# Kernel tuning notes

Measured on AMD Instinct MI355X. Metric: run time of the kernel, lower is better.

The kernel has to match this reference:

```python
import math
import jax, jax.numpy as jnp
import numpy as np

DIM = 1024
HEADS = 16
HEAD_DIM = DIM // HEADS
NEG = -10000.0


def setup_inputs() -> dict:
    key = jax.random.key(0)
    ks = jax.random.split(key, 9)
    B, S = 2, 2048
    s = 1.0 / math.sqrt(DIM)
    inp = {
        "x": jax.random.normal(ks[0], (B, S, DIM), dtype=jnp.float32),
        "Wq": jax.random.normal(ks[1], (DIM, DIM), dtype=jnp.float32) * s,
        "bq": jnp.zeros((DIM,), dtype=jnp.float32),
        "Wk": jax.random.normal(ks[2], (DIM, DIM), dtype=jnp.float32) * s,
        "bk": jnp.zeros((DIM,), dtype=jnp.float32),
        "Wv": jax.random.normal(ks[3], (DIM, DIM), dtype=jnp.float32) * s,
        "bv": jnp.zeros((DIM,), dtype=jnp.float32),
        "Wo": jax.random.normal(ks[4], (DIM, DIM), dtype=jnp.float32) * s,
        "bo": jnp.zeros((DIM,), dtype=jnp.float32),
    }
    return inp


def reference(x, Wq, bq, Wk, bk, Wv, bv, Wo, bo):
    B, S, D = x.shape
    q = x @ Wq + bq
    k = x @ Wk + bk
    v = x @ Wv + bv
    # [B, H, S, hd]
    def split_heads(t):
        return t.reshape(B, S, HEADS, HEAD_DIM).transpose(0, 2, 1, 3)
    q, k, v = split_heads(q), split_heads(k), split_heads(v)
    scores = jnp.einsum("bhqd,bhkd->bhqk", q, k) / math.sqrt(HEAD_DIM)
    causal = jnp.tril(jnp.ones((S, S), dtype=bool))  # [S, S]
    scores = jnp.where(causal[None, None], scores, NEG)
    probs = jax.nn.softmax(scores, axis=-1)
    ctx = jnp.einsum("bhqk,bhkd->bhqd", probs, v)  # [B, H, S, hd]
    ctx = ctx.transpose(0, 2, 1, 3).reshape(B, S, D)
    out = ctx @ Wo + bo
    return out
```

## Files before the change

kernel.cpp:

```cpp
#include <hip/hip_runtime.h>
#include <hip/hip_bf16.h>
#include <math.h>

#define DIMX 1024
#define HEADSX 16
#define HDX 64
#define BBX 2
#define SSX 2048
#define MMX (BBX*SSX)

typedef __bf16 bf16x8 __attribute__((ext_vector_type(8)));
typedef __bf16 bf16x4 __attribute__((ext_vector_type(4)));
typedef float  f32x4  __attribute__((ext_vector_type(4)));

#define NEGF (-1e30f)
#define QSCALE 0.18033688011112042f

static __device__ __forceinline__ void gload16(const void* g, void* l) {
  __builtin_amdgcn_global_load_lds(
      (const __attribute__((address_space(1))) unsigned int*)g,
      (__attribute__((address_space(3))) unsigned int*)l, 16, 0, 0);
}

__global__ __launch_bounds__(256) void k_prep(
    const float* __restrict__ x, const float* __restrict__ Wq,
    const float* __restrict__ Wk, const float* __restrict__ Wv,
    const float* __restrict__ Wo, __bf16* __restrict__ xb,
    __bf16* __restrict__ wqkvT, __bf16* __restrict__ woT) {
  const int bid = blockIdx.x;
  if (bid < 4096) {
    int i = (bid * 256 + threadIdx.x) * 4;
    float4 v = *(const float4*)&x[i];
    bf16x4 o = { (__bf16)v.x, (__bf16)v.y, (__bf16)v.z, (__bf16)v.w };
    *(bf16x4*)&xb[i] = o;
    return;
  }
  __shared__ __bf16 tile[64][65];
  const int wb = bid - 4096;
  const int mat = wb >> 8, t8 = wb & 255;
  const float* src = (mat == 0) ? Wq : (mat == 1) ? Wk : (mat == 2) ? Wv : Wo;
  __bf16* dst = (mat < 3) ? (wqkvT + (size_t)mat * DIMX * DIMX) : woT;
  const int tx = t8 & 15, ty = t8 >> 4;
  const int k0 = ty * 64, n0 = tx * 64;
  #pragma unroll
  for (int rep = 0; rep < 16; ++rep) {
    int idx = rep * 256 + threadIdx.x;
    int r = idx >> 6, c = idx & 63;
    tile[r][c] = (__bf16)src[(size_t)(k0 + r) * DIMX + n0 + c];
  }
  __syncthreads();
  #pragma unroll
  for (int rep = 0; rep < 16; ++rep) {
    int idx = rep * 256 + threadIdx.x;
    int r = idx >> 6, c = idx & 63;
    dst[(size_t)(n0 + r) * DIMX + k0 + c] = tile[c][r];
  }
}

__global__ __launch_bounds__(256) void k_gemm_qkv(
    const __bf16* __restrict__ A,
    const __bf16* __restrict__ Bt,
    const float* __restrict__ b0, const float* __restrict__ b1,
    const float* __restrict__ b2,
    __bf16* __restrict__ qb, __bf16* __restrict__ kb, __bf16* __restrict__ vtb) {
  constexpr int BK = 32, K = 1024;
  __shared__ __bf16 As[128 * BK];
  __shared__ __bf16 Bs[128 * BK];
  const int tid = threadIdx.x, lane = tid & 63, wave = tid >> 6;
  const int g = lane >> 4, r16 = lane & 15;
  const int wm = wave & 1, wn = wave >> 1;
  const int id = blockIdx.x;
  const int xcd = id & 7, j96 = id >> 3;
  const int m0 = (xcd * 4 + (j96 & 3)) * 128;
  const int n0 = (j96 >> 2) * 128;

  f32x4 acc[4][4] = {};

  for (int k0 = 0; k0 < K; k0 += BK) {
    __syncthreads();
    #pragma unroll
    for (int i = 0; i < 2; ++i) {
      int c = wave * 64 + lane + 256 * i;
      gload16(&A [(size_t)(m0 + (c >> 2)) * K + k0 + (c & 3) * 8],
              (char*)As + (size_t)(wave * 64 + 256 * i) * 16);
      gload16(&Bt[(size_t)(n0 + (c >> 2)) * K + k0 + (c & 3) * 8],
              (char*)Bs + (size_t)(wave * 64 + 256 * i) * 16);
    }
    __syncthreads();
    bf16x8 af[4], bfr[4];
    #pragma unroll
    for (int i = 0; i < 4; ++i)
      af[i]  = *(const bf16x8*)&As[(wm * 64 + i * 16 + r16) * BK + g * 8];
    #pragma unroll
    for (int j = 0; j < 4; ++j)
      bfr[j] = *(const bf16x8*)&Bs[(wn * 64 + j * 16 + r16) * BK + g * 8];
    #pragma unroll
    for (int i = 0; i < 4; ++i)
      #pragma unroll
      for (int j = 0; j < 4; ++j)
        acc[i][j] = __builtin_amdgcn_mfma_f32_16x16x32_bf16(af[i], bfr[j],
                                                            acc[i][j], 0, 0, 0);
  }

  #pragma unroll
  for (int i = 0; i < 4; ++i) {
    #pragma unroll
    for (int j = 0; j < 4; ++j) {
      #pragma unroll
      for (int r = 0; r < 4; ++r) {
        int m = m0 + wm * 64 + i * 16 + 4 * g + r;
        int n = n0 + wn * 64 + j * 16 + r16;
        float v = acc[i][j][r];
        int proj = n >> 10, w = n & 1023, h = w >> 6, d = w & 63;
        const float* bp = (proj == 0) ? b0 : (proj == 1) ? b1 : b2;
        v += bp[w];
        int b = m >> 11, s = m & 2047, bh = b * HEADSX + h;
        if (proj == 0)      qb [((size_t)bh * SSX + s) * HDX + d] =
                                (__bf16)(v * QSCALE);
        else if (proj == 1) kb [((size_t)bh * SSX + s) * HDX + d] = (__bf16)v;
        else                vtb[((size_t)bh * HDX + d) * SSX + s] = (__bf16)v;
      }
    }
  }
}

__global__ __launch_bounds__(256) void k_gemm_out(
    const __bf16* __restrict__ A,
    const __bf16* __restrict__ Bt,
    const float* __restrict__ bias, float* __restrict__ outf) {
  constexpr int BK = 32, K = 1024;
  __shared__ __bf16 As[128 * BK];
  __shared__ __bf16 Bs[64 * BK];
  const int tid = threadIdx.x, lane = tid & 63, wave = tid >> 6;
  const int g = lane >> 4, r16 = lane & 15;
  const int wm = wave & 1, wn = wave >> 1;
  const int id = blockIdx.x;
  const int xcd = id & 7, j64 = id >> 3;
  const int m0 = (xcd * 4 + (j64 & 3)) * 128;
  const int n0 = (j64 >> 2) * 64;

  f32x4 acc[4][2] = {};

  for (int k0 = 0; k0 < K; k0 += BK) {
    __syncthreads();
    #pragma unroll
    for (int i = 0; i < 2; ++i) {
      int c = wave * 64 + lane + 256 * i;
      gload16(&A [(size_t)(m0 + (c >> 2)) * K + k0 + (c & 3) * 8],
              (char*)As + (size_t)(wave * 64 + 256 * i) * 16);
    }
    {
      int c = tid;
      gload16(&Bt[(size_t)(n0 + (c >> 2)) * K + k0 + (c & 3) * 8],
              (char*)Bs + (size_t)(wave * 64) * 16);
    }
    __syncthreads();
    bf16x8 af[4], bfr[2];
    #pragma unroll
    for (int i = 0; i < 4; ++i)
      af[i]  = *(const bf16x8*)&As[(wm * 64 + i * 16 + r16) * BK + g * 8];
    #pragma unroll
    for (int j = 0; j < 2; ++j)
      bfr[j] = *(const bf16x8*)&Bs[(wn * 32 + j * 16 + r16) * BK + g * 8];
    #pragma unroll
    for (int i = 0; i < 4; ++i)
      #pragma unroll
      for (int j = 0; j < 2; ++j)
        acc[i][j] = __builtin_amdgcn_mfma_f32_16x16x32_bf16(af[i], bfr[j],
                                                            acc[i][j], 0, 0, 0);
  }

  #pragma unroll
  for (int i = 0; i < 4; ++i)
    #pragma unroll
    for (int j = 0; j < 2; ++j)
      #pragma unroll
      for (int r = 0; r < 4; ++r) {
        int m = m0 + wm * 64 + i * 16 + 4 * g + r;
        int n = n0 + wn * 32 + j * 16 + r16;
        outf[(size_t)m * DIMX + n] = acc[i][j][r] + bias[n];
      }
}

__global__ __launch_bounds__(256, 2) void k_attn(
    const __bf16* __restrict__ qb, const __bf16* __restrict__ kb,
    const __bf16* __restrict__ vtb, __bf16* __restrict__ ctxb) {
  const int tid = threadIdx.x;
  const int lane = tid & 63, wq = tid >> 6;
  const int g = lane >> 4, r16 = lane & 15;

  const int id = blockIdx.x;
  const int xcd = id & 7, idx = id >> 3;
  const int bh = xcd * 4 + (idx & 3);
  const int p  = idx >> 2;
  const int b = bh >> 4, h = bh & 15;

  const int ntL = p + 1, ntH = 32 - p;
  const int q0L = p * 64 + wq * 16;
  const int q0H = (31 - p) * 64 + wq * 16;

  const __bf16* Q  = qb  + (size_t)bh * SSX * HDX;
  const __bf16* Kp = kb  + (size_t)bh * SSX * HDX;
  const __bf16* Vt = vtb + (size_t)bh * HDX * SSX;

  __shared__ __bf16 Ks[4][64 * 64];
  __shared__ __bf16 Vs[4][64 * 64];
  __shared__ unsigned Pld[4][512];

  bf16x8 qfL[2], qfH[2];
  qfL[0] = *(const bf16x8*)&Q[(size_t)(q0L + r16) * HDX + g * 8];
  qfL[1] = *(const bf16x8*)&Q[(size_t)(q0L + r16) * HDX + 32 + g * 8];
  qfH[0] = *(const bf16x8*)&Q[(size_t)(q0H + r16) * HDX + g * 8];
  qfH[1] = *(const bf16x8*)&Q[(size_t)(q0H + r16) * HDX + 32 + g * 8];

  f32x4 accL[4] = {}, accH[4] = {};
  float mrunL = NEGF, lrunL = 0.f;
  float mrunH = NEGF, lrunH = 0.f;

  auto STAGE = [&](int t) {
    const int slot = t & 3;
    const int kv0 = t * 64;
    #pragma unroll
    for (int i = 0; i < 2; ++i) {
      int c = tid + 256 * i;
      int r = c >> 3;
      int cb = (c & 7) ^ (r & 7);
      gload16(&Kp[(size_t)(kv0 + r) * HDX + cb * 8],
              (char*)Ks[slot] + (size_t)(wq * 64 + 256 * i) * 16);
      gload16(&Vt[(size_t)r * SSX + kv0 + cb * 8],
              (char*)Vs[slot] + (size_t)(wq * 64 + 256 * i) * 16);
    }
  };

  auto SUBTILE = [&](const bf16x8* qf, f32x4* acc, float& mrun, float& lrun,
                     int qrow, bool last, int kv0, int slot) {
    f32x4 sac[4] = {};
    __builtin_amdgcn_s_setprio(1);
    #pragma unroll
    for (int kk = 0; kk < 2; ++kk)
      #pragma unroll
      for (int jj = 0; jj < 4; ++jj) {
        int rr = jj * 16 + r16;
        bf16x8 kf = *(const bf16x8*)
            &Ks[slot][rr * 64 + (((kk << 2) + g) ^ (rr & 7)) * 8];
        sac[jj] = __builtin_amdgcn_mfma_f32_16x16x32_bf16(kf, qf[kk], sac[jj],
                                                          0, 0, 0);
      }
    __builtin_amdgcn_s_setprio(0);

    float pv[4][4];
    float mt = NEGF;
    #pragma unroll
    for (int jj = 0; jj < 4; ++jj)
      #pragma unroll
      for (int r = 0; r < 4; ++r) {
        float s = sac[jj][r];
        if (last) {
          int kcol = kv0 + jj * 16 + 4 * g + r;
          s = (kcol > qrow) ? NEGF : s;
        }
        pv[jj][r] = s;
        mt = fmaxf(mt, s);
      }
    mt = fmaxf(mt, __shfl_xor(mt, 16));
    mt = fmaxf(mt, __shfl_xor(mt, 32));

    if (__any(mt > mrun)) {
      float mnew = fmaxf(mrun, mt);
      float fac = exp2f(mrun - mnew);
      mrun = mnew;
      lrun *= fac;
      #pragma unroll
      for (int j2 = 0; j2 < 4; ++j2)
        #pragma unroll
        for (int r = 0; r < 4; ++r)
          acc[j2][r] *= fac;
    }
    float rs = 0.f;
    #pragma unroll
    for (int jj = 0; jj < 4; ++jj)
      #pragma unroll
      for (int r = 0; r < 4; ++r) {
        float px = exp2f(pv[jj][r] - mrun);
        pv[jj][r] = px;
        rs += px;
      }
    lrun += rs;

    #pragma unroll
    for (int jj = 0; jj < 4; ++jj)
      #pragma unroll
      for (int rp = 0; rp < 2; ++rp) {
        unsigned w;
        asm("v_cvt_pk_bf16_f32 %0, %1, %2"
            : "=v"(w) : "v"(pv[jj][2 * rp]), "v"(pv[jj][2 * rp + 1]));
        int c = jj * 8 + g * 2 + rp;
        int addr = r16 * 32 + (((c >> 2) ^ (r16 & 7)) << 2) + (c & 3);
        Pld[wq][addr] = w;
      }

    bf16x8 pf[2];
    #pragma unroll
    for (int half = 0; half < 2; ++half) {
      int c = half * 16 + g * 4;
      int addr = r16 * 32 + (((c >> 2) ^ (r16 & 7)) << 2);
      pf[half] = *(const bf16x8*)&Pld[wq][addr];
    }
    __builtin_amdgcn_s_setprio(1);
    #pragma unroll
    for (int j2 = 0; j2 < 4; ++j2)
      #pragma unroll
      for (int half = 0; half < 2; ++half) {
        int dd = j2 * 16 + r16;
        bf16x8 vf = *(const bf16x8*)
            &Vs[slot][dd * 64 + (((half << 2) + g) ^ (dd & 7)) * 8];
        acc[j2] = __builtin_amdgcn_mfma_f32_16x16x32_bf16(vf, pf[half],
                                                          acc[j2], 0, 0, 0);
      }
    __builtin_amdgcn_s_setprio(0);
  };

  STAGE(0);
  if (ntH > 1) STAGE(1);
  __syncthreads();

  for (int t = 0; t < ntH; t += 2) {
    if (t + 2 < ntH) STAGE(t + 2);
    if (t + 3 < ntH) STAGE(t + 3);

    SUBTILE(qfH, accH, mrunH, lrunH, q0H + r16, t == ntH - 1, t * 64, t & 3);
    if (t < ntL)
      SUBTILE(qfL, accL, mrunL, lrunL, q0L + r16, t == ntL - 1, t * 64, t & 3);

    if (t + 1 < ntH) {
      SUBTILE(qfH, accH, mrunH, lrunH, q0H + r16, t + 1 == ntH - 1,
              (t + 1) * 64, (t + 1) & 3);
      if (t + 1 < ntL)
        SUBTILE(qfL, accL, mrunL, lrunL, q0L + r16, t + 1 == ntL - 1,
                (t + 1) * 64, (t + 1) & 3);
    }
    __syncthreads();
  }

  auto EPIL = [&](f32x4* acc, float lrun, int q0) {
    lrun += __shfl_xor(lrun, 16);
    lrun += __shfl_xor(lrun, 32);
    const float inv = 1.f / lrun;
    const int s = q0 + r16;
    #pragma unroll
    for (int j2 = 0; j2 < 4; ++j2)
      #pragma unroll
      for (int r = 0; r < 4; ++r) {
        int d = j2 * 16 + 4 * g + r;
        ctxb[((size_t)(b * SSX + s)) * DIMX + h * HDX + d] =
            (__bf16)(acc[j2][r] * inv);
      }
  };
  EPIL(accH, lrunH, q0H);
  EPIL(accL, lrunL, q0L);
}

extern "C" void kernel_launch(void* const* d_in, const int* in_sizes, int n_in,
                              void* d_out, int out_size, void* d_ws,
                              size_t ws_size, hipStream_t stream) {
  const float* x  = (const float*)d_in[0];
  const float* Wq = (const float*)d_in[1];
  const float* bq = (const float*)d_in[2];
  const float* Wk = (const float*)d_in[3];
  const float* bk = (const float*)d_in[4];
  const float* Wv = (const float*)d_in[5];
  const float* bv = (const float*)d_in[6];
  const float* Wo = (const float*)d_in[7];
  const float* bo = (const float*)d_in[8];
  float* out = (float*)d_out;

  char* ws = (char*)d_ws;
  __bf16* xb    = (__bf16*)(ws);
  __bf16* wqkvT = (__bf16*)(ws + ((size_t)8  << 20));
  __bf16* woT   = (__bf16*)(ws + ((size_t)14 << 20));
  __bf16* qb    = (__bf16*)(ws + ((size_t)16 << 20));
  __bf16* kb    = (__bf16*)(ws + ((size_t)24 << 20));
  __bf16* vtb   = (__bf16*)(ws + ((size_t)32 << 20));
  __bf16* ctxb  = xb;

  k_prep<<<5120, 256, 0, stream>>>(x, Wq, Wk, Wv, Wo, xb, wqkvT, woT);
  k_gemm_qkv<<<768, 256, 0, stream>>>(xb, wqkvT, bq, bk, bv, qb, kb, vtb);
  k_attn<<<512, 256, 0, stream>>>(qb, kb, vtb, ctxb);
  k_gemm_out<<<512, 256, 0, stream>>>(ctxb, woT, bo, out);
}
```

Measured before the change: 120.7 us.

## Double-buffer GEMM K-loops, simplify attention staging, widen x conversion

Both projection GEMMs now load the next K slice into a second LDS buffer while the current slice feeds the MFMAs, so each iteration needs one barrier instead of two. The attention kernel moves from a 4-slot, two-tile-per-iteration K/V ring to a 2-slot double buffer processing one tile per iteration, cutting LDS use but adding a barrier per tile. The x-to-bf16 conversion handles 8 elements per thread, halving its block count. The attention change lowers prefetch depth, which could expose more load latency, in exchange for better occupancy.

```diff
diff --git a/kernel.cpp b/kernel.cpp
--- a/kernel.cpp
+++ b/kernel.cpp
@@ -28,15 +28,17 @@
     const float* __restrict__ Wo, __bf16* __restrict__ xb,
     __bf16* __restrict__ wqkvT, __bf16* __restrict__ woT) {
   const int bid = blockIdx.x;
-  if (bid < 4096) {
-    int i = (bid * 256 + threadIdx.x) * 4;
-    float4 v = *(const float4*)&x[i];
-    bf16x4 o = { (__bf16)v.x, (__bf16)v.y, (__bf16)v.z, (__bf16)v.w };
-    *(bf16x4*)&xb[i] = o;
+  if (bid < 2048) {
+    int i = (bid * 256 + threadIdx.x) * 8;
+    float4 v0 = *(const float4*)&x[i];
+    float4 v1 = *(const float4*)&x[i + 4];
+    bf16x8 o = { (__bf16)v0.x, (__bf16)v0.y, (__bf16)v0.z, (__bf16)v0.w,
+                 (__bf16)v1.x, (__bf16)v1.y, (__bf16)v1.z, (__bf16)v1.w };
+    *(bf16x8*)&xb[i] = o;
     return;
   }
   __shared__ __bf16 tile[64][65];
-  const int wb = bid - 4096;
+  const int wb = bid - 2048;
   const int mat = wb >> 8, t8 = wb & 255;
   const float* src = (mat == 0) ? Wq : (mat == 1) ? Wk : (mat == 2) ? Wv : Wo;
   __bf16* dst = (mat < 3) ? (wqkvT + (size_t)mat * DIMX * DIMX) : woT;
@@ -64,8 +66,8 @@
     const float* __restrict__ b2,
     __bf16* __restrict__ qb, __bf16* __restrict__ kb, __bf16* __restrict__ vtb) {
   constexpr int BK = 32, K = 1024;
-  __shared__ __bf16 As[128 * BK];
-  __shared__ __bf16 Bs[128 * BK];
+  __shared__ __bf16 As[2][128 * BK];
+  __shared__ __bf16 Bs[2][128 * BK];
   const int tid = threadIdx.x, lane = tid & 63, wave = tid >> 6;
   const int g = lane >> 4, r16 = lane & 15;
   const int wm = wave & 1, wn = wave >> 1;
@@ -74,26 +76,31 @@
   const int m0 = (xcd * 4 + (j96 & 3)) * 128;
   const int n0 = (j96 >> 2) * 128;
 
-  f32x4 acc[4][4] = {};
-
-  for (int k0 = 0; k0 < K; k0 += BK) {
-    __syncthreads();
+  auto STAGE = [&](int buf, int k0) {
     #pragma unroll
     for (int i = 0; i < 2; ++i) {
       int c = wave * 64 + lane + 256 * i;
       gload16(&A [(size_t)(m0 + (c >> 2)) * K + k0 + (c & 3) * 8],
-              (char*)As + (size_t)(wave * 64 + 256 * i) * 16);
+              (char*)As[buf] + (size_t)(wave * 64 + 256 * i) * 16);
       gload16(&Bt[(size_t)(n0 + (c >> 2)) * K + k0 + (c & 3) * 8],
-              (char*)Bs + (size_t)(wave * 64 + 256 * i) * 16);
-    }
+              (char*)Bs[buf] + (size_t)(wave * 64 + 256 * i) * 16);
+    }
+  };
+
+  f32x4 acc[4][4] = {};
+
+  STAGE(0, 0);
+  int cur = 0;
+  for (int k0 = 0; k0 < K; k0 += BK, cur ^= 1) {
     __syncthreads();
+    if (k0 + BK < K) STAGE(cur ^ 1, k0 + BK);
     bf16x8 af[4], bfr[4];
     #pragma unroll
     for (int i = 0; i < 4; ++i)
-      af[i]  = *(const bf16x8*)&As[(wm * 64 + i * 16 + r16) * BK + g * 8];
+      af[i]  = *(const bf16x8*)&As[cur][(wm * 64 + i * 16 + r16) * BK + g * 8];
     #pragma unroll
     for (int j = 0; j < 4; ++j)
-      bfr[j] = *(const bf16x8*)&Bs[(wn * 64 + j * 16 + r16) * BK + g * 8];
+      bfr[j] = *(const bf16x8*)&Bs[cur][(wn * 64 + j * 16 + r16) * BK + g * 8];
     #pragma unroll
     for (int i = 0; i < 4; ++i)
       #pragma unroll
@@ -129,8 +136,8 @@
     const __bf16* __restrict__ Bt,
     const float* __restrict__ bias, float* __restrict__ outf) {
   constexpr int BK = 32, K = 1024;
-  __shared__ __bf16 As[128 * BK];
-  __shared__ __bf16 Bs[64 * BK];
+  __shared__ __bf16 As[2][128 * BK];
+  __shared__ __bf16 Bs[2][64 * BK];
   const int tid = threadIdx.x, lane = tid & 63, wave = tid >> 6;
   const int g = lane >> 4, r16 = lane & 15;
   const int wm = wave & 1, wn = wave >> 1;
@@ -139,29 +146,34 @@
   const int m0 = (xcd * 4 + (j64 & 3)) * 128;
   const int n0 = (j64 >> 2) * 64;
 
-  f32x4 acc[4][2] = {};
-
-  for (int k0 = 0; k0 < K; k0 += BK) {
-    __syncthreads();
+  auto STAGE = [&](int buf, int k0) {
     #pragma unroll
     for (int i = 0; i < 2; ++i) {
       int c = wave * 64 + lane + 256 * i;
       gload16(&A [(size_t)(m0 + (c >> 2)) * K + k0 + (c & 3) * 8],
-              (char*)As + (size_t)(wave * 64 + 256 * i) * 16);
+              (char*)As[buf] + (size_t)(wave * 64 + 256 * i) * 16);
     }
     {
       int c = tid;
       gload16(&Bt[(size_t)(n0 + (c >> 2)) * K + k0 + (c & 3) * 8],
-              (char*)Bs + (size_t)(wave * 64) * 16);
-    }
+              (char*)Bs[buf] + (size_t)(wave * 64) * 16);
+    }
+  };
+
+  f32x4 acc[4][2] = {};
+
+  STAGE(0, 0);
+  int cur = 0;
+  for (int k0 = 0; k0 < K; k0 += BK, cur ^= 1) {
     __syncthreads();
+    if (k0 + BK < K) STAGE(cur ^ 1, k0 + BK);
     bf16x8 af[4], bfr[2];
     #pragma unroll
     for (int i = 0; i < 4; ++i)
-      af[i]  = *(const bf16x8*)&As[(wm * 64 + i * 16 + r16) * BK + g * 8];
+      af[i]  = *(const bf16x8*)&As[cur][(wm * 64 + i * 16 + r16) * BK + g * 8];
     #pragma unroll
     for (int j = 0; j < 2; ++j)
-      bfr[j] = *(const bf16x8*)&Bs[(wn * 32 + j * 16 + r16) * BK + g * 8];
+      bfr[j] = *(const bf16x8*)&Bs[cur][(wn * 32 + j * 16 + r16) * BK + g * 8];
     #pragma unroll
     for (int i = 0; i < 4; ++i)
       #pragma unroll
@@ -203,8 +215,8 @@
   const __bf16* Kp = kb  + (size_t)bh * SSX * HDX;
   const __bf16* Vt = vtb + (size_t)bh * HDX * SSX;
 
-  __shared__ __bf16 Ks[4][64 * 64];
-  __shared__ __bf16 Vs[4][64 * 64];
+  __shared__ __bf16 Ks[2][64 * 64];
+  __shared__ __bf16 Vs[2][64 * 64];
   __shared__ unsigned Pld[4][512];
 
   bf16x8 qfL[2], qfH[2];
@@ -217,8 +229,7 @@
   float mrunL = NEGF, lrunL = 0.f;
   float mrunH = NEGF, lrunH = 0.f;
 
-  auto STAGE = [&](int t) {
-    const int slot = t & 3;
+  auto STAGE = [&](int buf, int t) {
     const int kv0 = t * 64;
     #pragma unroll
     for (int i = 0; i < 2; ++i) {
@@ -226,14 +237,14 @@
       int r = c >> 3;
       int cb = (c & 7) ^ (r & 7);
       gload16(&Kp[(size_t)(kv0 + r) * HDX + cb * 8],
-              (char*)Ks[slot] + (size_t)(wq * 64 + 256 * i) * 16);
+              (char*)Ks[buf] + (size_t)(wq * 64 + 256 * i) * 16);
       gload16(&Vt[(size_t)r * SSX + kv0 + cb * 8],
-              (char*)Vs[slot] + (size_t)(wq * 64 + 256 * i) * 16);
+              (char*)Vs[buf] + (size_t)(wq * 64 + 256 * i) * 16);
     }
   };
 
   auto SUBTILE = [&](const bf16x8* qf, f32x4* acc, float& mrun, float& lrun,
-                     int qrow, bool last, int kv0, int slot) {
+                     int qrow, bool last, int kv0, int cur) {
     f32x4 sac[4] = {};
     __builtin_amdgcn_s_setprio(1);
     #pragma unroll
@@ -242,7 +253,7 @@
       for (int jj = 0; jj < 4; ++jj) {
         int rr = jj * 16 + r16;
         bf16x8 kf = *(const bf16x8*)
-            &Ks[slot][rr * 64 + (((kk << 2) + g) ^ (rr & 7)) * 8];
+            &Ks[cur][rr * 64 + (((kk << 2) + g) ^ (rr & 7)) * 8];
         sac[jj] = __builtin_amdgcn_mfma_f32_16x16x32_bf16(kf, qf[kk], sac[jj],
                                                           0, 0, 0);
       }
@@ -313,32 +324,25 @@
       for (int half = 0; half < 2; ++half) {
         int dd = j2 * 16 + r16;
         bf16x8 vf = *(const bf16x8*)
-            &Vs[slot][dd * 64 + (((half << 2) + g) ^ (dd & 7)) * 8];
+            &Vs[cur][dd * 64 + (((half << 2) + g) ^ (dd & 7)) * 8];
         acc[j2] = __builtin_amdgcn_mfma_f32_16x16x32_bf16(vf, pf[half],
                                                           acc[j2], 0, 0, 0);
       }
     __builtin_amdgcn_s_setprio(0);
   };
 
-  STAGE(0);
-  if (ntH > 1) STAGE(1);
+  STAGE(0, 0);
   __syncthreads();
 
-  for (int t = 0; t < ntH; t += 2) {
-    if (t + 2 < ntH) STAGE(t + 2);
-    if (t + 3 < ntH) STAGE(t + 3);
-
-    SUBTILE(qfH, accH, mrunH, lrunH, q0H + r16, t == ntH - 1, t * 64, t & 3);
+  for (int t = 0; t < ntH; ++t) {
+    const int cur = t & 1;
+    if (t + 1 < ntH) STAGE(cur ^ 1, t + 1);
+    const int kv0 = t * 64;
+
+    SUBTILE(qfH, accH, mrunH, lrunH, q0H + r16, t == ntH - 1, kv0, cur);
     if (t < ntL)
-      SUBTILE(qfL, accL, mrunL, lrunL, q0L + r16, t == ntL - 1, t * 64, t & 3);
-
-    if (t + 1 < ntH) {
-      SUBTILE(qfH, accH, mrunH, lrunH, q0H + r16, t + 1 == ntH - 1,
-              (t + 1) * 64, (t + 1) & 3);
-      if (t + 1 < ntL)
-        SUBTILE(qfL, accL, mrunL, lrunL, q0L + r16, t + 1 == ntL - 1,
-                (t + 1) * 64, (t + 1) & 3);
-    }
+      SUBTILE(qfL, accL, mrunL, lrunL, q0L + r16, t == ntL - 1, kv0, cur);
+
     __syncthreads();
   }
 
@@ -383,7 +387,7 @@
   __bf16* vtb   = (__bf16*)(ws + ((size_t)32 << 20));
   __bf16* ctxb  = xb;
 
-  k_prep<<<5120, 256, 0, stream>>>(x, Wq, Wk, Wv, Wo, xb, wqkvT, woT);
+  k_prep<<<3072, 256, 0, stream>>>(x, Wq, Wk, Wv, Wo, xb, wqkvT, woT);
   k_gemm_qkv<<<768, 256, 0, stream>>>(xb, wqkvT, bq, bk, bv, qb, kb, vtb);
   k_attn<<<512, 256, 0, stream>>>(qb, kb, vtb, ctxb);
   k_gemm_out<<<512, 256, 0, stream>>>(ctxb, woT, bo, out);
```

New measurement: 121.9 us. Within noise of the previous version (+1.0%).
